# Kernel tuning notes

Measured on AMD Instinct MI355X. Metric: run time of the kernel, lower is better.

The kernel has to match this reference:

```python
import jax, jax.numpy as jnp
import numpy as np

IN_CAPS, OUT_CAPS, OUT_DIM = 32, 10, 16


def squash(s):
    # s: [B, out_caps, out_dim]
    sq = jnp.sum(s * s, axis=2)              # [B, out_caps]
    mod = jnp.sqrt(sq)
    scale = sq / (1.0 + sq) / mod            # matches torch: sqrmod/(1+sqrmod)/mod
    return scale[..., None] * s


def setup_inputs() -> dict:
    key = jax.random.key(0)
    k1, k2 = jax.random.split(key)
    B, in_dim = 4096, 288
    caps_output = jax.random.normal(k1, (B, IN_CAPS, in_dim), dtype=jnp.float32)
    # W initialized uniform(-1/32, 1/32) in the original; scale randn similarly small
    W = jax.random.uniform(k2, (IN_CAPS, in_dim, OUT_CAPS * OUT_DIM),
                           dtype=jnp.float32, minval=-1.0 / 32, maxval=1.0 / 32)
    b = jnp.zeros((IN_CAPS, OUT_CAPS), dtype=jnp.float32)
    return {"caps_output": caps_output, "W": W, "b": b}


def reference(caps_output, W, b):
    B = caps_output.shape[0]
    # caps_output.unsqueeze(2).matmul(W): per-input-capsule matmul
    u = jnp.einsum('bni,nio->bno', caps_output, W)          # [B, 32, 160]
    u = u.reshape(B, IN_CAPS, OUT_CAPS, OUT_DIM)            # [B, 32, 10, 16]

    c = jax.nn.softmax(b, axis=1)                           # [32, 10]
    s = jnp.einsum('no,bnod->bod', c, u)                    # [B, 10, 16]
    v = squash(s)

    b_batch = jnp.broadcast_to(b, (B, IN_CAPS, OUT_CAPS))
    for _ in range(3):
        # agreement: <u_predict, v>
        b_batch = b_batch + jnp.einsum('bnod,bod->bno', u, v)
        c = jax.nn.softmax(b_batch, axis=-1)                # [B, 32, 10]
        s = jnp.einsum('bno,bnod->bod', c, u)
        v = squash(s)
    return v
```

## Files before the change

### kernel.cpp

```cpp
#include <hip/hip_runtime.h>
#include <hip/hip_bf16.h>

#define IN_CAPS 32
#define OUT_CAPS 10
#define OUT_DIM 16
#define NOUT 160
#define KDIM 288
#define BATCH 4096
#define KSTEPS 9
#define CTILES 10
#define USTR 169

typedef __bf16 bf16x8 __attribute__((ext_vector_type(8)));
typedef float  f32x4  __attribute__((ext_vector_type(4)));

__global__ __launch_bounds__(256) void prep_w(const float* __restrict__ W,
                                              __bf16* __restrict__ Wf) {
    int f = blockIdx.x * 256 + threadIdx.x;
    int j    = f & 7;
    int l    = (f >> 3) & 63;
    int rest = f >> 9;
    int c    = rest % CTILES;
    int tnk  = rest / CTILES;
    int ks   = tnk % KSTEPS;
    int n    = tnk / KSTEPS;
    int k    = ks * 32 + (l >> 4) * 8 + j;
    int col  = c * 16 + (l & 15);
    Wf[f] = (__bf16)W[(n * KDIM + k) * NOUT + col];
}

__global__ __launch_bounds__(256, 4) void gemm_u(const float* __restrict__ caps,
                                                 const __bf16* __restrict__ Wf,
                                                 __bf16* __restrict__ u) {
    const int n       = blockIdx.y;
    const int wave    = threadIdx.x >> 6;
    const int lane    = threadIdx.x & 63;
    const int rowbase = blockIdx.x * 128 + wave * 32;
    const int lm      = lane & 15;
    const int lk      = lane >> 4;

    f32x4 acc[2][CTILES];
#pragma unroll
    for (int mt = 0; mt < 2; ++mt)
#pragma unroll
        for (int ct = 0; ct < CTILES; ++ct)
            acc[mt][ct] = (f32x4){0.f, 0.f, 0.f, 0.f};

    const __bf16* wfn = Wf + (size_t)n * (KSTEPS * CTILES * 512);

    for (int ks = 0; ks < KSTEPS; ++ks) {
        bf16x8 afr[2];
#pragma unroll
        for (int mt = 0; mt < 2; ++mt) {
            const float* src = caps + (size_t)(rowbase + mt * 16 + lm) * (IN_CAPS * KDIM)
                                    + n * KDIM + ks * 32 + lk * 8;
            f32x4 x0 = *(const f32x4*)(src);
            f32x4 x1 = *(const f32x4*)(src + 4);
            bf16x8 a;
            a[0] = (__bf16)x0[0]; a[1] = (__bf16)x0[1];
            a[2] = (__bf16)x0[2]; a[3] = (__bf16)x0[3];
            a[4] = (__bf16)x1[0]; a[5] = (__bf16)x1[1];
            a[6] = (__bf16)x1[2]; a[7] = (__bf16)x1[3];
            afr[mt] = a;
        }
        const __bf16* wks = wfn + (size_t)ks * (CTILES * 512) + lane * 8;
#pragma unroll
        for (int ct = 0; ct < CTILES; ++ct) {
            bf16x8 bfr = *(const bf16x8*)(wks + ct * 512);
#pragma unroll
            for (int mt = 0; mt < 2; ++mt)
                acc[mt][ct] = __builtin_amdgcn_mfma_f32_16x16x32_bf16(afr[mt], bfr, acc[mt][ct], 0, 0, 0);
        }
    }

#pragma unroll
    for (int mt = 0; mt < 2; ++mt)
#pragma unroll
        for (int ct = 0; ct < CTILES; ++ct)
#pragma unroll
            for (int r = 0; r < 4; ++r) {
                int row = rowbase + mt * 16 + lk * 4 + r;
                int col = ct * 16 + lm;
                u[((size_t)row * IN_CAPS + n) * NOUT + col] = (__bf16)acc[mt][ct][r];
            }
}

__global__ __launch_bounds__(256) void routing(const __bf16* __restrict__ u,
                                               const float* __restrict__ bbias,
                                               float* __restrict__ out) {
    __shared__ float ul[2][IN_CAPS * USTR];
    __shared__ float bl[2][IN_CAPS * OUT_CAPS];
    __shared__ float cs[2][IN_CAPS * OUT_CAPS];
    __shared__ float ss[2][NOUT];
    __shared__ float vs[2][NOUT];
    __shared__ float scale_s[2][OUT_CAPS];

    const int t  = threadIdx.x;
    const int gb = t >> 7;
    const int g  = t & 127;
    const size_t b = (size_t)blockIdx.x * 2 + gb;
    const __bf16* ub = u + b * (IN_CAPS * NOUT);

    for (int cc = g; cc < 640; cc += 128) {
        int n = cc / 20;
        int rem = cc - n * 20;
        uint4 raw = *(const uint4*)(ub + cc * 8);
        bf16x8 bv = __builtin_bit_cast(bf16x8, raw);
#pragma unroll
        for (int j = 0; j < 8; ++j) ul[gb][n * USTR + rem * 8 + j] = (float)bv[j];
    }
    for (int p = g; p < IN_CAPS * OUT_CAPS; p += 128) bl[gb][p] = bbias[p];
    __syncthreads();

    for (int it = 0; it < 4; ++it) {
        if (it > 0) {
            for (int p = g; p < IN_CAPS * OUT_CAPS; p += 128) {
                int n = p & 31;
                int o = p >> 5;
                float a = 0.f;
#pragma unroll
                for (int d = 0; d < 16; ++d)
                    a += ul[gb][n * USTR + o * 16 + d] * vs[gb][o * 16 + d];
                bl[gb][n * 10 + o] += a;
            }
            __syncthreads();
        }
        if (g < IN_CAPS) {
            float m = bl[gb][g * 10];
#pragma unroll
            for (int o = 1; o < 10; ++o) m = fmaxf(m, bl[gb][g * 10 + o]);
            float e[10];
            float sum = 0.f;
#pragma unroll
            for (int o = 0; o < 10; ++o) { e[o] = __expf(bl[gb][g * 10 + o] - m); sum += e[o]; }
            float inv = 1.0f / sum;
#pragma unroll
            for (int o = 0; o < 10; ++o) cs[gb][g * 10 + o] = e[o] * inv;
        }
        __syncthreads();
        for (int p = g; p < NOUT; p += 128) {
            int o = p >> 4;
            float acc = 0.f;
#pragma unroll
            for (int n = 0; n < IN_CAPS; ++n)
                acc += cs[gb][n * 10 + o] * ul[gb][n * USTR + p];
            ss[gb][p] = acc;
        }
        __syncthreads();
        if (g < OUT_CAPS) {
            float sq = 0.f;
#pragma unroll
            for (int d = 0; d < 16; ++d) { float x = ss[gb][g * 16 + d]; sq += x * x; }
            scale_s[gb][g] = sq / ((1.0f + sq) * sqrtf(sq));
        }
        __syncthreads();
        for (int p = g; p < NOUT; p += 128) vs[gb][p] = scale_s[gb][p >> 4] * ss[gb][p];
        __syncthreads();
    }

    for (int p = g; p < NOUT; p += 128) out[b * NOUT + p] = vs[gb][p];
}

extern "C" void kernel_launch(void* const* d_in, const int* in_sizes, int n_in,
                              void* d_out, int out_size, void* d_ws, size_t ws_size,
                              hipStream_t stream) {
    const float* caps  = (const float*)d_in[0];
    const float* W     = (const float*)d_in[1];
    const float* bbias = (const float*)d_in[2];
    float* out = (float*)d_out;

    __bf16* Wf = (__bf16*)d_ws;
    __bf16* u  = (__bf16*)((char*)d_ws + 2949120);

    prep_w<<<dim3(5760), dim3(256), 0, stream>>>(W, Wf);
    gemm_u<<<dim3(32, 32), dim3(256), 0, stream>>>(caps, Wf, u);
    routing<<<dim3(BATCH / 2), dim3(256), 0, stream>>>(u, bbias, out);
}
```

Measured before the change: 86.73 us.

## Store u in MFMA fragment order, prefetch A, and route four samples per block

The GEMM now writes u in its native MFMA accumulator layout as packed 16-byte stores instead of scattered 2-byte stores. The routing kernel reads that layout back and unpacks it into bf16 shared memory. The change also prefetches the next K-step of the A operand to overlap global loads with MFMA work. Routing now handles four batch samples per block, with 64 threads each, which halves the grid and the shared-memory footprint per sample. The cost is more complex gather indexing, more bf16-to-float conversions in the inner loops, and less per-sample parallelism in routing.

```diff
diff --git a/kernel.cpp b/kernel.cpp
--- a/kernel.cpp
+++ b/kernel.cpp
@@ -3,13 +3,12 @@
 
 #define IN_CAPS 32
 #define OUT_CAPS 10
-#define OUT_DIM 16
 #define NOUT 160
 #define KDIM 288
 #define BATCH 4096
 #define KSTEPS 9
 #define CTILES 10
-#define USTR 169
+#define STR2 162
 
 typedef __bf16 bf16x8 __attribute__((ext_vector_type(8)));
 typedef float  f32x4  __attribute__((ext_vector_type(4)));
@@ -29,15 +28,15 @@
     Wf[f] = (__bf16)W[(n * KDIM + k) * NOUT + col];
 }
 
-__global__ __launch_bounds__(256, 4) void gemm_u(const float* __restrict__ caps,
-                                                 const __bf16* __restrict__ Wf,
-                                                 __bf16* __restrict__ u) {
-    const int n       = blockIdx.y;
-    const int wave    = threadIdx.x >> 6;
-    const int lane    = threadIdx.x & 63;
-    const int rowbase = blockIdx.x * 128 + wave * 32;
-    const int lm      = lane & 15;
-    const int lk      = lane >> 4;
+__global__ __launch_bounds__(256) void gemm_u(const float* __restrict__ caps,
+                                              const __bf16* __restrict__ Wf,
+                                              uint4* __restrict__ up) {
+    const int n    = blockIdx.y;
+    const int wave = threadIdx.x >> 6;
+    const int lane = threadIdx.x & 63;
+    const int rw   = blockIdx.x * 4 + wave;
+    const int lm   = lane & 15;
+    const int lk   = lane >> 4;
 
     f32x4 acc[2][CTILES];
 #pragma unroll
@@ -46,119 +45,140 @@
         for (int ct = 0; ct < CTILES; ++ct)
             acc[mt][ct] = (f32x4){0.f, 0.f, 0.f, 0.f};
 
-    const __bf16* wfn = Wf + (size_t)n * (KSTEPS * CTILES * 512);
+    const float* a0 = caps + (size_t)(rw * 32 + lm) * (IN_CAPS * KDIM) + n * KDIM + lk * 8;
+    const float* a1 = a0 + (size_t)16 * (IN_CAPS * KDIM);
+    const __bf16* wfn = Wf + (size_t)n * (KSTEPS * CTILES * 512) + lane * 8;
+
+    f32x4 pre[4];
+    pre[0] = *(const f32x4*)(a0);
+    pre[1] = *(const f32x4*)(a0 + 4);
+    pre[2] = *(const f32x4*)(a1);
+    pre[3] = *(const f32x4*)(a1 + 4);
 
     for (int ks = 0; ks < KSTEPS; ++ks) {
         bf16x8 afr[2];
 #pragma unroll
         for (int mt = 0; mt < 2; ++mt) {
-            const float* src = caps + (size_t)(rowbase + mt * 16 + lm) * (IN_CAPS * KDIM)
-                                    + n * KDIM + ks * 32 + lk * 8;
-            f32x4 x0 = *(const f32x4*)(src);
-            f32x4 x1 = *(const f32x4*)(src + 4);
             bf16x8 a;
-            a[0] = (__bf16)x0[0]; a[1] = (__bf16)x0[1];
-            a[2] = (__bf16)x0[2]; a[3] = (__bf16)x0[3];
-            a[4] = (__bf16)x1[0]; a[5] = (__bf16)x1[1];
-            a[6] = (__bf16)x1[2]; a[7] = (__bf16)x1[3];
+            a[0] = (__bf16)pre[2*mt][0]; a[1] = (__bf16)pre[2*mt][1];
+            a[2] = (__bf16)pre[2*mt][2]; a[3] = (__bf16)pre[2*mt][3];
+            a[4] = (__bf16)pre[2*mt+1][0]; a[5] = (__bf16)pre[2*mt+1][1];
+            a[6] = (__bf16)pre[2*mt+1][2]; a[7] = (__bf16)pre[2*mt+1][3];
             afr[mt] = a;
         }
-        const __bf16* wks = wfn + (size_t)ks * (CTILES * 512) + lane * 8;
+        if (ks + 1 < KSTEPS) {
+            const float* n0 = a0 + (ks + 1) * 32;
+            const float* n1 = a1 + (ks + 1) * 32;
+            pre[0] = *(const f32x4*)(n0);
+            pre[1] = *(const f32x4*)(n0 + 4);
+            pre[2] = *(const f32x4*)(n1);
+            pre[3] = *(const f32x4*)(n1 + 4);
+        }
+        const __bf16* wks = wfn + (size_t)ks * (CTILES * 512);
 #pragma unroll
         for (int ct = 0; ct < CTILES; ++ct) {
             bf16x8 bfr = *(const bf16x8*)(wks + ct * 512);
-#pragma unroll
-            for (int mt = 0; mt < 2; ++mt)
-                acc[mt][ct] = __builtin_amdgcn_mfma_f32_16x16x32_bf16(afr[mt], bfr, acc[mt][ct], 0, 0, 0);
+            acc[0][ct] = __builtin_amdgcn_mfma_f32_16x16x32_bf16(afr[0], bfr, acc[0][ct], 0, 0, 0);
+            acc[1][ct] = __builtin_amdgcn_mfma_f32_16x16x32_bf16(afr[1], bfr, acc[1][ct], 0, 0, 0);
         }
     }
 
+    const size_t cbase = (((size_t)n * 128 + rw) * 2) * 5 * 64 + lane;
 #pragma unroll
     for (int mt = 0; mt < 2; ++mt)
 #pragma unroll
-        for (int ct = 0; ct < CTILES; ++ct)
+        for (int p = 0; p < 5; ++p) {
+            bf16x8 pk;
 #pragma unroll
-            for (int r = 0; r < 4; ++r) {
-                int row = rowbase + mt * 16 + lk * 4 + r;
-                int col = ct * 16 + lm;
-                u[((size_t)row * IN_CAPS + n) * NOUT + col] = (__bf16)acc[mt][ct][r];
-            }
+            for (int j = 0; j < 8; ++j)
+                pk[j] = (__bf16)acc[mt][2 * p + (j >> 2)][j & 3];
+            up[cbase + ((size_t)mt * 5 + p) * 64] = __builtin_bit_cast(uint4, pk);
+        }
 }
 
-__global__ __launch_bounds__(256) void routing(const __bf16* __restrict__ u,
+__global__ __launch_bounds__(256) void routing(const uint4* __restrict__ up,
                                                const float* __restrict__ bbias,
                                                float* __restrict__ out) {
-    __shared__ float ul[2][IN_CAPS * USTR];
-    __shared__ float bl[2][IN_CAPS * OUT_CAPS];
-    __shared__ float cs[2][IN_CAPS * OUT_CAPS];
-    __shared__ float ss[2][NOUT];
-    __shared__ float vs[2][NOUT];
-    __shared__ float scale_s[2][OUT_CAPS];
+    __shared__ __bf16 ul[4][IN_CAPS * STR2];
+    __shared__ float  bl[4][IN_CAPS * OUT_CAPS];
+    __shared__ float  cs[4][IN_CAPS * OUT_CAPS];
+    __shared__ float  ss[4][NOUT];
+    __shared__ float  vs[4][NOUT];
+    __shared__ float  scale_s[4][16];
 
     const int t  = threadIdx.x;
-    const int gb = t >> 7;
-    const int g  = t & 127;
-    const size_t b = (size_t)blockIdx.x * 2 + gb;
-    const __bf16* ub = u + b * (IN_CAPS * NOUT);
+    const int b0 = blockIdx.x * 4;
+    const int rw = b0 >> 5;
+    const int mt = (b0 >> 4) & 1;
+    const int lk = (b0 >> 2) & 3;
 
-    for (int cc = g; cc < 640; cc += 128) {
-        int n = cc / 20;
-        int rem = cc - n * 20;
-        uint4 raw = *(const uint4*)(ub + cc * 8);
-        bf16x8 bv = __builtin_bit_cast(bf16x8, raw);
+    for (int c = t; c < 2560; c += 256) {
+        int n   = c / 80;
+        int rem = c - n * 80;
+        int p   = rem >> 4;
+        int lm  = rem & 15;
+        size_t idx = ((((size_t)n * 128 + rw) * 2 + mt) * 5 + p) * 64 + lk * 16 + lm;
+        bf16x8 v = __builtin_bit_cast(bf16x8, up[idx]);
 #pragma unroll
-        for (int j = 0; j < 8; ++j) ul[gb][n * USTR + rem * 8 + j] = (float)bv[j];
+        for (int j = 0; j < 8; ++j) {
+            int ct = 2 * p + (j >> 2);
+            int rr = j & 3;
+            ul[rr][n * STR2 + ct * 16 + lm] = v[j];
+        }
     }
-    for (int p = g; p < IN_CAPS * OUT_CAPS; p += 128) bl[gb][p] = bbias[p];
+    const int grp = t >> 6;
+    const int g   = t & 63;
+    for (int pp = g; pp < IN_CAPS * OUT_CAPS; pp += 64) bl[grp][pp] = bbias[pp];
     __syncthreads();
 
     for (int it = 0; it < 4; ++it) {
         if (it > 0) {
-            for (int p = g; p < IN_CAPS * OUT_CAPS; p += 128) {
-                int n = p & 31;
-                int o = p >> 5;
+            for (int pp = g; pp < IN_CAPS * OUT_CAPS; pp += 64) {
+                int n = pp & 31;
+                int o = pp >> 5;
                 float a = 0.f;
 #pragma unroll
                 for (int d = 0; d < 16; ++d)
-                    a += ul[gb][n * USTR + o * 16 + d] * vs[gb][o * 16 + d];
-                bl[gb][n * 10 + o] += a;
+                    a += (float)ul[grp][n * STR2 + o * 16 + d] * vs[grp][o * 16 + d];
+                bl[grp][n * 10 + o] += a;
             }
             __syncthreads();
         }
         if (g < IN_CAPS) {
-            float m = bl[gb][g * 10];
+            float m = bl[grp][g * 10];
 #pragma unroll
-            for (int o = 1; o < 10; ++o) m = fmaxf(m, bl[gb][g * 10 + o]);
+            for (int o = 1; o < 10; ++o) m = fmaxf(m, bl[grp][g * 10 + o]);
             float e[10];
             float sum = 0.f;
 #pragma unroll
-            for (int o = 0; o < 10; ++o) { e[o] = __expf(bl[gb][g * 10 + o] - m); sum += e[o]; }
+            for (int o = 0; o < 10; ++o) { e[o] = __expf(bl[grp][g * 10 + o] - m); sum += e[o]; }
             float inv = 1.0f / sum;
 #pragma unroll
-            for (int o = 0; o < 10; ++o) cs[gb][g * 10 + o] = e[o] * inv;
+            for (int o = 0; o < 10; ++o) cs[grp][g * 10 + o] = e[o] * inv;
         }
         __syncthreads();
-        for (int p = g; p < NOUT; p += 128) {
+        for (int p = g; p < NOUT; p += 64) {
             int o = p >> 4;
-            float acc = 0.f;
+            float a = 0.f;
 #pragma unroll
             for (int n = 0; n < IN_CAPS; ++n)
-                acc += cs[gb][n * 10 + o] * ul[gb][n * USTR + p];
-            ss[gb][p] = acc;
+                a += cs[grp][n * 10 + o] * (float)ul[grp][n * STR2 + p];
+            ss[grp][p] = a;
         }
         __syncthreads();
         if (g < OUT_CAPS) {
             float sq = 0.f;
 #pragma unroll
-            for (int d = 0; d < 16; ++d) { float x = ss[gb][g * 16 + d]; sq += x * x; }
-            scale_s[gb][g] = sq / ((1.0f + sq) * sqrtf(sq));
+            for (int d = 0; d < 16; ++d) { float x = ss[grp][g * 16 + d]; sq += x * x; }
+            scale_s[grp][g] = sq / ((1.0f + sq) * sqrtf(sq));
         }
         __syncthreads();
-        for (int p = g; p < NOUT; p += 128) vs[gb][p] = scale_s[gb][p >> 4] * ss[gb][p];
+        for (int p = g; p < NOUT; p += 64) vs[grp][p] = scale_s[grp][p >> 4] * ss[grp][p];
         __syncthreads();
     }
 
-    for (int p = g; p < NOUT; p += 128) out[b * NOUT + p] = vs[gb][p];
+    for (int p = g; p < NOUT; p += 64)
+        out[(size_t)(b0 + grp) * NOUT + p] = vs[grp][p];
 }
 
 extern "C" void kernel_launch(void* const* d_in, const int* in_sizes, int n_in,
@@ -170,9 +190,9 @@
     float* out = (float*)d_out;
 
     __bf16* Wf = (__bf16*)d_ws;
-    __bf16* u  = (__bf16*)((char*)d_ws + 2949120);
+    uint4*  up = (uint4*)((char*)d_ws + 2949120);
 
     prep_w<<<dim3(5760), dim3(256), 0, stream>>>(W, Wf);
-    gemm_u<<<dim3(32, 32), dim3(256), 0, stream>>>(caps, Wf, u);
-    routing<<<dim3(BATCH / 2), dim3(256), 0, stream>>>(u, bbias, out);
+    gemm_u<<<dim3(32, 32), dim3(256), 0, stream>>>(caps, Wf, up);
+    routing<<<dim3(BATCH / 4), dim3(256), 0, stream>>>(up, bbias, out);
 }
```

After: 82.22 us. 5.2% less time.
